# Kernel optimization log

Measured on AMD Instinct MI355X. Metric: run time of the kernel, lower is better.

Reference implementation:

```python
import jax, jax.numpy as jnp
import numpy as np

B, H, W = 8, 640, 640
NUM_INST = 16  # upper bound on instance ids; segment reduce handles absent ids


def _bce(p, t):
    # torch BCELoss clamps log terms at -100
    lp = jnp.clip(jnp.log(p), -100.0)
    l1p = jnp.clip(jnp.log1p(-p), -100.0)
    return -(t * lp + (1.0 - t) * l1p)


def setup_inputs() -> dict:
    key = jax.random.key(0)
    k1, k2, k3, k4 = jax.random.split(key, 4)
    preds = jax.random.uniform(k1, (B, 2, H, W), dtype=jnp.float32,
                               minval=1e-4, maxval=1.0 - 1e-4)
    conf = jax.random.bernoulli(k2, 0.3, (B, H, W)).astype(jnp.float32)
    overlap = jax.random.bernoulli(k3, 0.1, (B, H, W)).astype(jnp.float32)
    inst = jax.random.randint(k4, (B, H, W), 0, NUM_INST, dtype=jnp.int32)
    inds = jnp.arange(B, dtype=jnp.int64) if jax.config.jax_enable_x64 else jnp.arange(B, dtype=jnp.int32)
    return {"preds": preds, "conf": conf, "inst": inst,
            "overlap": overlap, "inds": inds}


def reference(preds, conf, inst, overlap, inds):
    p1 = preds[:, 0]
    p2 = preds[:, 1]
    and_preds = p1 * p2
    and_loss_map = _bce(and_preds, overlap)            # [B,H,W]
    or_loss = _bce(jnp.maximum(p1, p2), conf).mean()
    and_overlap = and_preds * overlap
    op1 = jnp.maximum(p1, and_overlap)
    op2 = jnpp = jnp.maximum(p2, and_overlap)

    b, h, w = p1.shape
    # per-(sample, instance-id) segment reduce replacing the python loops.
    # MSELoss(bop*mask, mask)/sum(mask) == segment-mean of (op-1)^2 over the mask.
    seg = (jnp.arange(b, dtype=jnp.int32)[:, None, None] * NUM_INST + inst).reshape(-1)
    e1 = ((op1 - 1.0) ** 2).reshape(-1)
    e2 = ((op2 - 1.0) ** 2).reshape(-1)
    nseg = b * NUM_INST
    cnt = jax.ops.segment_sum(jnp.ones_like(e1), seg, num_segments=nseg).reshape(b, NUM_INST)
    s1 = jax.ops.segment_sum(e1, seg, num_segments=nseg).reshape(b, NUM_INST)
    s2 = jax.ops.segment_sum(e2, seg, num_segments=nseg).reshape(b, NUM_INST)
    present = cnt > 0
    safe_cnt = jnp.where(present, cnt, 1.0)
    d1 = s1 / safe_cnt
    d2 = s2 / safe_cnt
    # min(d1,d2) - max(d1,d2) + 1 == 1 - |d1 - d2|, only for present keys
    per_key = jnp.where(present, 1.0 - jnp.abs(d1 - d2), 0.0)
    nkeys = present.sum(axis=1).astype(p1.dtype)       # torch.unique count per sample
    inst_loss = (per_key.sum(axis=1) / nkeys).mean()

    pos = (conf == 1).astype(p1.dtype)
    neg = (conf == 0).astype(p1.dtype)
    and_loss = (and_loss_map * pos).sum() / pos.sum() + (and_loss_map * neg).sum() / neg.sum()

    return 0.5 * and_loss + 0.25 * or_loss + 0.25 * inst_loss
```

## Files before the change

kernel.cpp:

```cpp
#include <hip/hip_runtime.h>

#define BB 8
#define HH 640
#define WW 640
#define HWN (HH * WW)
#define NUM_INST 16
#define NBLK 256
#define NBLK_TOT (NBLK * BB)
#define THREADS 256
#define NV 36
#define NVEC (HWN / 4)
#define VPB (NVEC / NBLK)


__device__ __forceinline__ void process_pixel(
    float p1, float p2, float c, float t, int k,
    float* s12, unsigned* cnt_s,
    float& lgPos, float& lgAll, float& lgOr, float& accCnt)
{
    float andp = p1 * p2;
    bool tpos = (t != 0.0f);
    bool cpos = (c != 0.0f);
    float argA = tpos ? andp : (1.0f - andp);
    float lg = __log2f(argA);
    lgAll += lg;
    lgPos = fmaf(c, lg, lgPos);
    accCnt += c;
    float mx = fmaxf(p1, p2);
    float argO = cpos ? mx : (1.0f - mx);
    lgOr += __log2f(argO);
    float ao = t * andp;
    float d1 = fmaxf(p1, ao) - 1.0f;
    float d2 = fmaxf(p2, ao) - 1.0f;
    float e12 = (d1 - d2) * (d1 + d2);
    #pragma unroll
    for (int j = 0; j < NUM_INST; ++j) {
        bool m = (k == j);
        s12[j] += m ? e12 : 0.0f;
        cnt_s[j] += (unsigned)__popcll(__ballot(m));
    }
}

__global__ __launch_bounds__(THREADS, 8) void overlap_main_kernel(
    const float* __restrict__ preds, const float* __restrict__ conf,
    const int* __restrict__ inst, const float* __restrict__ overlap,
    float* __restrict__ ws)
{
    const int b   = blockIdx.y;
    const int tid = threadIdx.x;

    const float4* p1v = (const float4*)(preds + (size_t)b * 2 * HWN);
    const float4* p2v = p1v + NVEC;
    const float4* cv  = (const float4*)(conf    + (size_t)b * HWN);
    const float4* tv  = (const float4*)(overlap + (size_t)b * HWN);
    const int4*   kv  = (const int4*)(inst      + (size_t)b * HWN);

    float s12[NUM_INST];
    unsigned cnt_s[NUM_INST];
    #pragma unroll
    for (int j = 0; j < NUM_INST; ++j) { s12[j] = 0.0f; cnt_s[j] = 0u; }
    float lgPos = 0.0f, lgAll = 0.0f, lgOr = 0.0f, accCnt = 0.0f;

    const int lim = (blockIdx.x + 1) * VPB;
    for (int i = blockIdx.x * VPB + tid; i < lim; i += THREADS) {
        float4 A  = p1v[i];
        float4 Bv = p2v[i];
        float4 C  = cv[i];
        float4 T  = tv[i];
        int4   K  = kv[i];
        process_pixel(A.x, Bv.x, C.x, T.x, K.x, s12, cnt_s, lgPos, lgAll, lgOr, accCnt);
        process_pixel(A.y, Bv.y, C.y, T.y, K.y, s12, cnt_s, lgPos, lgAll, lgOr, accCnt);
        process_pixel(A.z, Bv.z, C.z, T.z, K.z, s12, cnt_s, lgPos, lgAll, lgOr, accCnt);
        process_pixel(A.w, Bv.w, C.w, T.w, K.w, s12, cnt_s, lgPos, lgAll, lgOr, accCnt);
    }

    float fv[20];
    #pragma unroll
    for (int j = 0; j < NUM_INST; ++j) fv[j] = s12[j];
    fv[16] = lgPos; fv[17] = lgAll; fv[18] = lgOr; fv[19] = accCnt;
    #pragma unroll
    for (int s = 32; s > 0; s >>= 1) {
        #pragma unroll
        for (int v = 0; v < 20; ++v) fv[v] += __shfl_xor(fv[v], s, 64);
    }

    __shared__ float wsum[4][NV];
    const int wave = tid >> 6;
    const int lane = tid & 63;
    if (lane == 0) {
        #pragma unroll
        for (int j = 0; j < NUM_INST; ++j) {
            wsum[wave][j]      = fv[j];
            wsum[wave][16 + j] = (float)cnt_s[j];
        }
        wsum[wave][32] = fv[16];
        wsum[wave][33] = fv[17];
        wsum[wave][34] = fv[18];
        wsum[wave][35] = fv[19];
    }
    __syncthreads();
    if (tid < NV) {
        float s = wsum[0][tid] + wsum[1][tid] + wsum[2][tid] + wsum[3][tid];
        if (tid >= 32 && tid < 35)
            s = -0.69314718055994530942f * s;
        int g = blockIdx.y * NBLK + blockIdx.x;
        ws[tid * NBLK_TOT + g] = s;
    }
}

__global__ __launch_bounds__(640) void overlap_finalize_kernel(
    const float* __restrict__ ws, float* __restrict__ out)
{
    __shared__ float seg2[BB][NV][2];
    __shared__ float seg[BB][NV];
    __shared__ float perkey[BB][NUM_INST];
    __shared__ float pres[BB][NUM_INST];
    __shared__ float binst[BB];
    const int t = threadIdx.x;

    if (t < BB * NV * 2) {
        int idx = t >> 1, half = t & 1;
        int b = idx / NV, v = idx - (idx / NV) * NV;
        const float4* p = (const float4*)(ws + v * NBLK_TOT + b * NBLK) + half * (NBLK / 8);
        float4 s4 = {0.0f, 0.0f, 0.0f, 0.0f};
        #pragma unroll 8
        for (int i = 0; i < NBLK / 8; ++i) {
            float4 q = p[i];
            s4.x += q.x; s4.y += q.y; s4.z += q.z; s4.w += q.w;
        }
        seg2[b][v][half] = (s4.x + s4.y) + (s4.z + s4.w);
    }
    __syncthreads();

    if (t < BB * NV) {
        int b = t / NV, v = t - (t / NV) * NV;
        seg[b][v] = seg2[b][v][0] + seg2[b][v][1];
    }
    __syncthreads();

    if (t < BB * NUM_INST) {
        int b = t >> 4, k = t & 15;
        float c = seg[b][16 + k];
        bool present = c > 0.0f;
        float sc = present ? c : 1.0f;
        perkey[b][k] = present ? (1.0f - fabsf(seg[b][k]) / sc) : 0.0f;
        pres[b][k]   = present ? 1.0f : 0.0f;
    }
    __syncthreads();

    if (t < BB) {
        float s = 0.0f, nk = 0.0f;
        for (int k = 0; k < NUM_INST; ++k) { s += perkey[t][k]; nk += pres[t][k]; }
        binst[t] = s / nk;
    }
    __syncthreads();

    if (t == 0) {
        float instLoss = 0.0f, posS = 0.0f, allS = 0.0f, orS = 0.0f, posC = 0.0f;
        for (int b = 0; b < BB; ++b) {
            instLoss += binst[b];
            posS += seg[b][32];
            allS += seg[b][33];
            orS  += seg[b][34];
            posC += seg[b][35];
        }
        instLoss *= (1.0f / (float)BB);
        const float N = (float)BB * (float)HWN;
        float negS = allS - posS;
        float andLoss = posS / posC + negS / (N - posC);
        float orLoss  = orS / N;
        out[0] = 0.5f * andLoss + 0.25f * orLoss + 0.25f * instLoss;
    }
}

extern "C" void kernel_launch(void* const* d_in, const int* in_sizes, int n_in,
                              void* d_out, int out_size, void* d_ws, size_t ws_size,
                              hipStream_t stream) {
    const float* preds   = (const float*)d_in[0];
    const float* conf    = (const float*)d_in[1];
    const int*   inst    = (const int*)d_in[2];
    const float* overlap = (const float*)d_in[3];
    float* ws  = (float*)d_ws;
    float* out = (float*)d_out;

    dim3 grid(NBLK, BB);
    overlap_main_kernel<<<grid, THREADS, 0, stream>>>(preds, conf, inst, overlap, ws);
    overlap_finalize_kernel<<<1, 640, 0, stream>>>(ws, out);
}
```

Baseline: 117.2 us.

## Front-load all per-thread loads with fewer, larger blocks and simplify finalize

The grid is resized to 64 blocks per sample with 320 threads, so each thread handles exactly five vector iterations. All five iterations of input loads are issued into registers before any compute, to raise memory-level parallelism. The finalize kernel now reduces a quarter as many partials per segment in a single pass, dropping one shared stage and a barrier. The cost is lower occupancy and higher register use per thread.

```diff
diff --git a/kernel.cpp b/kernel.cpp
--- a/kernel.cpp
+++ b/kernel.cpp
@@ -5,12 +5,14 @@
 #define WW 640
 #define HWN (HH * WW)
 #define NUM_INST 16
-#define NBLK 256
+#define NBLK 64
 #define NBLK_TOT (NBLK * BB)
-#define THREADS 256
+#define THREADS 320
+#define NWAVE (THREADS / 64)
 #define NV 36
 #define NVEC (HWN / 4)
 #define VPB (NVEC / NBLK)
+#define ITER (VPB / THREADS)
 
 
 __device__ __forceinline__ void process_pixel(
@@ -41,13 +43,14 @@
     }
 }
 
-__global__ __launch_bounds__(THREADS, 8) void overlap_main_kernel(
+__global__ __launch_bounds__(THREADS, 4) void overlap_main_kernel(
     const float* __restrict__ preds, const float* __restrict__ conf,
     const int* __restrict__ inst, const float* __restrict__ overlap,
     float* __restrict__ ws)
 {
     const int b   = blockIdx.y;
     const int tid = threadIdx.x;
+    const int bs  = blockIdx.x * VPB;
 
     const float4* p1v = (const float4*)(preds + (size_t)b * 2 * HWN);
     const float4* p2v = p1v + NVEC;
@@ -55,23 +58,30 @@
     const float4* tv  = (const float4*)(overlap + (size_t)b * HWN);
     const int4*   kv  = (const int4*)(inst      + (size_t)b * HWN);
 
+    float4 A[ITER], Bv[ITER], C[ITER], T[ITER];
+    int4   K[ITER];
+    #pragma unroll
+    for (int it = 0; it < ITER; ++it) {
+        int i = bs + it * THREADS + tid;
+        A[it]  = p1v[i];
+        Bv[it] = p2v[i];
+        C[it]  = cv[i];
+        T[it]  = tv[i];
+        K[it]  = kv[i];
+    }
+
     float s12[NUM_INST];
     unsigned cnt_s[NUM_INST];
     #pragma unroll
     for (int j = 0; j < NUM_INST; ++j) { s12[j] = 0.0f; cnt_s[j] = 0u; }
     float lgPos = 0.0f, lgAll = 0.0f, lgOr = 0.0f, accCnt = 0.0f;
 
-    const int lim = (blockIdx.x + 1) * VPB;
-    for (int i = blockIdx.x * VPB + tid; i < lim; i += THREADS) {
-        float4 A  = p1v[i];
-        float4 Bv = p2v[i];
-        float4 C  = cv[i];
-        float4 T  = tv[i];
-        int4   K  = kv[i];
-        process_pixel(A.x, Bv.x, C.x, T.x, K.x, s12, cnt_s, lgPos, lgAll, lgOr, accCnt);
-        process_pixel(A.y, Bv.y, C.y, T.y, K.y, s12, cnt_s, lgPos, lgAll, lgOr, accCnt);
-        process_pixel(A.z, Bv.z, C.z, T.z, K.z, s12, cnt_s, lgPos, lgAll, lgOr, accCnt);
-        process_pixel(A.w, Bv.w, C.w, T.w, K.w, s12, cnt_s, lgPos, lgAll, lgOr, accCnt);
+    #pragma unroll
+    for (int it = 0; it < ITER; ++it) {
+        process_pixel(A[it].x, Bv[it].x, C[it].x, T[it].x, K[it].x, s12, cnt_s, lgPos, lgAll, lgOr, accCnt);
+        process_pixel(A[it].y, Bv[it].y, C[it].y, T[it].y, K[it].y, s12, cnt_s, lgPos, lgAll, lgOr, accCnt);
+        process_pixel(A[it].z, Bv[it].z, C[it].z, T[it].z, K[it].z, s12, cnt_s, lgPos, lgAll, lgOr, accCnt);
+        process_pixel(A[it].w, Bv[it].w, C[it].w, T[it].w, K[it].w, s12, cnt_s, lgPos, lgAll, lgOr, accCnt);
     }
 
     float fv[20];
@@ -84,7 +94,7 @@
         for (int v = 0; v < 20; ++v) fv[v] += __shfl_xor(fv[v], s, 64);
     }
 
-    __shared__ float wsum[4][NV];
+    __shared__ float wsum[NWAVE][NV];
     const int wave = tid >> 6;
     const int lane = tid & 63;
     if (lane == 0) {
@@ -100,7 +110,9 @@
     }
     __syncthreads();
     if (tid < NV) {
-        float s = wsum[0][tid] + wsum[1][tid] + wsum[2][tid] + wsum[3][tid];
+        float s = 0.0f;
+        #pragma unroll
+        for (int w = 0; w < NWAVE; ++w) s += wsum[w][tid];
         if (tid >= 32 && tid < 35)
             s = -0.69314718055994530942f * s;
         int g = blockIdx.y * NBLK + blockIdx.x;
@@ -108,33 +120,25 @@
     }
 }
 
-__global__ __launch_bounds__(640) void overlap_finalize_kernel(
+__global__ __launch_bounds__(320) void overlap_finalize_kernel(
     const float* __restrict__ ws, float* __restrict__ out)
 {
-    __shared__ float seg2[BB][NV][2];
     __shared__ float seg[BB][NV];
     __shared__ float perkey[BB][NUM_INST];
     __shared__ float pres[BB][NUM_INST];
     __shared__ float binst[BB];
     const int t = threadIdx.x;
 
-    if (t < BB * NV * 2) {
-        int idx = t >> 1, half = t & 1;
-        int b = idx / NV, v = idx - (idx / NV) * NV;
-        const float4* p = (const float4*)(ws + v * NBLK_TOT + b * NBLK) + half * (NBLK / 8);
+    if (t < BB * NV) {
+        int b = t / NV, v = t - (t / NV) * NV;
+        const float4* p = (const float4*)(ws + v * NBLK_TOT + b * NBLK);
         float4 s4 = {0.0f, 0.0f, 0.0f, 0.0f};
-        #pragma unroll 8
-        for (int i = 0; i < NBLK / 8; ++i) {
+        #pragma unroll
+        for (int i = 0; i < NBLK / 4; ++i) {
             float4 q = p[i];
             s4.x += q.x; s4.y += q.y; s4.z += q.z; s4.w += q.w;
         }
-        seg2[b][v][half] = (s4.x + s4.y) + (s4.z + s4.w);
-    }
-    __syncthreads();
-
-    if (t < BB * NV) {
-        int b = t / NV, v = t - (t / NV) * NV;
-        seg[b][v] = seg2[b][v][0] + seg2[b][v][1];
+        seg[b][v] = (s4.x + s4.y) + (s4.z + s4.w);
     }
     __syncthreads();
 
@@ -185,5 +189,5 @@
 
     dim3 grid(NBLK, BB);
     overlap_main_kernel<<<grid, THREADS, 0, stream>>>(preds, conf, inst, overlap, ws);
-    overlap_finalize_kernel<<<1, 640, 0, stream>>>(ws, out);
+    overlap_finalize_kernel<<<1, 320, 0, stream>>>(ws, out);
 }
```

New measurement: 116.4 us. Within noise of the previous version (-0.7%).
